# Kernel optimization log

Hardware: AMD Instinct MI355X
Metric: run time of the kernel (lower is better)

## Reference

```python
import jax, jax.numpy as jnp
import numpy as np

EPS = 1e-12  # torch F.normalize default eps


def _l2norm(x):
    n = jnp.linalg.norm(x, axis=-1, keepdims=True)
    return x / jnp.maximum(n, EPS)


def setup_inputs() -> dict:
    key = jax.random.key(0)
    k1, k2 = jax.random.split(key)
    B, D = 8192, 1024
    img_emb = jax.random.normal(k1, (B, D), dtype=jnp.float32)
    txt_emb = jax.random.normal(k2, (B, D), dtype=jnp.float32)
    t_prime = jnp.asarray(np.log(1.0 / 0.1), dtype=jnp.float32)  # log(1/temperature_init)
    bias = jnp.asarray(-10.0, dtype=jnp.float32)
    return {"img_emb": img_emb, "txt_emb": txt_emb, "t_prime": t_prime, "bias": bias}


def reference(img_emb, txt_emb, t_prime, bias):
    img = _l2norm(img_emb)
    txt = _l2norm(txt_emb)
    t = jnp.minimum(jnp.exp(t_prime), 100.0)
    logits = jnp.einsum('id,jd->ij', img, txt) * t + bias  # [B, B]
    B = img.shape[0]
    # STANDARD mode: labels = 2*I - 1
    labels = 2.0 * jnp.eye(B, dtype=logits.dtype) - 1.0
    loss = -jnp.sum(jax.nn.log_sigmoid(labels * logits)) / B
    return loss
```

## Files before the change

kernel.cpp:

```cpp
#include <hip/hip_runtime.h>
#include <hip/hip_bf16.h>

#define B_SZ 8192
#define D_SZ 1024

typedef __attribute__((ext_vector_type(4))) float floatx4;
typedef __attribute__((ext_vector_type(8))) int   int8v;
typedef __attribute__((ext_vector_type(4))) int   int4v;

__device__ __forceinline__ void glds16(const void* g, void* l) {
    __builtin_amdgcn_global_load_lds(
        (const __attribute__((address_space(1))) void*)g,
        (__attribute__((address_space(3))) void*)l, 16, 0, 0);
}

__global__ __launch_bounds__(256) void norm_cast_fp8(
    const float* __restrict__ img, const float* __restrict__ txt,
    unsigned char* __restrict__ imgQ, unsigned char* __restrict__ txtQ)
{
    const int lane = threadIdx.x & 63;
    int w = blockIdx.x * 4 + (threadIdx.x >> 6);
    const float* src; unsigned char* dst;
    if (w < B_SZ) { src = img + (size_t)w * D_SZ; dst = imgQ + (size_t)w * D_SZ; }
    else { w -= B_SZ; src = txt + (size_t)w * D_SZ; dst = txtQ + (size_t)w * D_SZ; }

    float4 v[4];
    float ss = 0.0f;
    #pragma unroll
    for (int i = 0; i < 4; ++i) {
        v[i] = ((const float4*)src)[lane + 64 * i];
        ss += v[i].x*v[i].x + v[i].y*v[i].y + v[i].z*v[i].z + v[i].w*v[i].w;
    }
    #pragma unroll
    for (int off = 1; off < 64; off <<= 1) ss += __shfl_xor(ss, off, 64);
    const float scale = 1.0f / fmaxf(sqrtf(ss), 1e-12f);

    #pragma unroll
    for (int i = 0; i < 4; ++i) {
        int packed = 0;
        packed = __builtin_amdgcn_cvt_pk_fp8_f32(v[i].x * scale, v[i].y * scale, packed, false);
        packed = __builtin_amdgcn_cvt_pk_fp8_f32(v[i].z * scale, v[i].w * scale, packed, true);
        ((int*)dst)[lane + 64 * i] = packed;
    }
}

__global__ __launch_bounds__(256, 3) void siglip_gemm_loss_fp8(
    const unsigned char* __restrict__ A,
    const unsigned char* __restrict__ Bt,
    const float* __restrict__ tp, const float* __restrict__ bp,
    float* __restrict__ out)
{
    __shared__ __align__(16) unsigned char As[2][128 * 64];
    __shared__ __align__(16) unsigned char Bs[2][128 * 64];

    const int tid  = threadIdx.x;
    const int lane = tid & 63;
    const int wave = tid >> 6;
    const int wm = wave & 1, wn = wave >> 1;
    const int bi = blockIdx.x * 128;
    const int bj = blockIdx.y * 128;
    const int quad = lane >> 4;
    const int l16  = lane & 15;

    floatx4 acc[4][4];
    #pragma unroll
    for (int i = 0; i < 4; ++i)
        #pragma unroll
        for (int j = 0; j < 4; ++j)
            acc[i][j] = (floatx4){0.f, 0.f, 0.f, 0.f};

    auto stage = [&](int k0) {
        #pragma unroll
        for (int it = 0; it < 2; ++it) {
            int s = tid + it * 256;
            int row = s >> 2, p = s & 3;
            int g = p ^ ((row >> 1) & 3);
            const unsigned char* ga = A  + ((size_t)(bi + row) * D_SZ + k0 + g * 16);
            const unsigned char* gb = Bt + ((size_t)(bj + row) * D_SZ + k0 + g * 16);
            glds16(ga,      As[0] + s * 16);
            glds16(ga + 64, As[1] + s * 16);
            glds16(gb,      Bs[0] + s * 16);
            glds16(gb + 64, Bs[1] + s * 16);
        }
    };

    const int sw = (l16 >> 1) & 3;
    const int hsel = quad >> 1;
    const int q2 = (quad & 1) * 2;
    const int p0 = (q2    ) ^ sw;
    const int p1 = (q2 + 1) ^ sw;

    stage(0);

    for (int kk = 0; kk < D_SZ / 128; ++kk) {
        __syncthreads();

        int8v af[4], bf[4];
        #pragma unroll
        for (int mt = 0; mt < 4; ++mt) {
            int r = wm * 64 + mt * 16 + l16;
            int4v lo = *(const int4v*)(As[hsel] + r * 64 + p0 * 16);
            int4v hi = *(const int4v*)(As[hsel] + r * 64 + p1 * 16);
            af[mt][0]=lo[0]; af[mt][1]=lo[1]; af[mt][2]=lo[2]; af[mt][3]=lo[3];
            af[mt][4]=hi[0]; af[mt][5]=hi[1]; af[mt][6]=hi[2]; af[mt][7]=hi[3];
        }
        #pragma unroll
        for (int nt = 0; nt < 4; ++nt) {
            int r = wn * 64 + nt * 16 + l16;
            int4v lo = *(const int4v*)(Bs[hsel] + r * 64 + p0 * 16);
            int4v hi = *(const int4v*)(Bs[hsel] + r * 64 + p1 * 16);
            bf[nt][0]=lo[0]; bf[nt][1]=lo[1]; bf[nt][2]=lo[2]; bf[nt][3]=lo[3];
            bf[nt][4]=hi[0]; bf[nt][5]=hi[1]; bf[nt][6]=hi[2]; bf[nt][7]=hi[3];
        }

        __syncthreads();

        if (kk + 1 < D_SZ / 128)
            stage((kk + 1) * 128);

        #pragma unroll
        for (int mt = 0; mt < 4; ++mt)
            #pragma unroll
            for (int nt = 0; nt < 4; ++nt)
                acc[mt][nt] = __builtin_amdgcn_mfma_scale_f32_16x16x128_f8f6f4(
                    af[mt], bf[nt], acc[mt][nt],
                    0, 0,
                    0, 127,
                    0, 127);
    }

    const float t    = fminf(__expf(tp[0]), 100.0f);
    const float bias = bp[0];
    float lsum = 0.0f;
    #pragma unroll
    for (int mt = 0; mt < 4; ++mt) {
        #pragma unroll
        for (int nt = 0; nt < 4; ++nt) {
            const int jj = bj + wn * 64 + nt * 16 + l16;
            #pragma unroll
            for (int r = 0; r < 4; ++r) {
                const int ii = bi + wm * 64 + mt * 16 + quad * 4 + r;
                float logit = fmaf(acc[mt][nt][r], t, bias);
                float z = (ii == jj) ? logit : -logit;
                float e = __expf(-fabsf(z));
                lsum += fmaxf(-z, 0.0f) + __logf(1.0f + e);
            }
        }
    }
    #pragma unroll
    for (int off = 32; off > 0; off >>= 1) lsum += __shfl_down(lsum, off, 64);

    __shared__ float red[4];
    if (lane == 0) red[wave] = lsum;
    __syncthreads();
    if (tid == 0)
        atomicAdd(out, (red[0] + red[1] + red[2] + red[3]) * (1.0f / (float)B_SZ));
}

extern "C" void kernel_launch(void* const* d_in, const int* in_sizes, int n_in,
                              void* d_out, int out_size, void* d_ws, size_t ws_size,
                              hipStream_t stream) {
    const float* img = (const float*)d_in[0];
    const float* txt = (const float*)d_in[1];
    const float* tp  = (const float*)d_in[2];
    const float* bp  = (const float*)d_in[3];
    float* out = (float*)d_out;

    unsigned char* imgQ = (unsigned char*)d_ws;
    unsigned char* txtQ = imgQ + (size_t)B_SZ * D_SZ;

    hipMemsetAsync(out, 0, sizeof(float), stream);
    norm_cast_fp8<<<(2 * B_SZ) / 4, 256, 0, stream>>>(img, txt, imgQ, txtQ);
    dim3 grid(B_SZ / 128, B_SZ / 128);
    siglip_gemm_loss_fp8<<<grid, 256, 0, stream>>>(imgQ, txtQ, tp, bp, out);
}
```

Baseline: 192.3 us.

## Enlarge GEMM tile to 256x128, double-buffer A, fold output zeroing into norm kernel

The fused GEMM+loss kernel now computes a 256x128 output tile per block, with each wave holding an 8x4 grid of MFMA accumulators. A fragments are streamed from LDS inside the MFMA loop, and the A tile is double-buffered in LDS. The goal is more reuse of each B fragment and fewer global loads per FLOP. The launch bound drops to 2 blocks per SM to fit the larger register and LDS footprint, and the grid is halved. The separate memset is removed and the output is zeroed inside the norm kernel, which saves one launch.

After: 229.7 us. +19.5%, slower.

```diff
diff --git a/kernel.cpp b/kernel.cpp
--- a/kernel.cpp
+++ b/kernel.cpp
@@ -16,8 +16,11 @@
 
 __global__ __launch_bounds__(256) void norm_cast_fp8(
     const float* __restrict__ img, const float* __restrict__ txt,
-    unsigned char* __restrict__ imgQ, unsigned char* __restrict__ txtQ)
+    unsigned char* __restrict__ imgQ, unsigned char* __restrict__ txtQ,
+    float* __restrict__ out)
 {
+    if (blockIdx.x == 0 && threadIdx.x == 0) *out = 0.0f;
+
     const int lane = threadIdx.x & 63;
     int w = blockIdx.x * 4 + (threadIdx.x >> 6);
     const float* src; unsigned char* dst;
@@ -44,102 +47,111 @@
     }
 }
 
-__global__ __launch_bounds__(256, 3) void siglip_gemm_loss_fp8(
+__global__ __launch_bounds__(256, 2) void siglip_gemm_loss_fp8(
     const unsigned char* __restrict__ A,
     const unsigned char* __restrict__ Bt,
     const float* __restrict__ tp, const float* __restrict__ bp,
     float* __restrict__ out)
 {
-    __shared__ __align__(16) unsigned char As[2][128 * 64];
+    __shared__ __align__(16) unsigned char As[2][2][256 * 64];
     __shared__ __align__(16) unsigned char Bs[2][128 * 64];
 
     const int tid  = threadIdx.x;
     const int lane = tid & 63;
     const int wave = tid >> 6;
     const int wm = wave & 1, wn = wave >> 1;
-    const int bi = blockIdx.x * 128;
+    const int bi = blockIdx.x * 256;
     const int bj = blockIdx.y * 128;
     const int quad = lane >> 4;
     const int l16  = lane & 15;
 
-    floatx4 acc[4][4];
+    floatx4 acc[8][4];
     #pragma unroll
-    for (int i = 0; i < 4; ++i)
+    for (int i = 0; i < 8; ++i)
         #pragma unroll
         for (int j = 0; j < 4; ++j)
             acc[i][j] = (floatx4){0.f, 0.f, 0.f, 0.f};
 
-    auto stage = [&](int k0) {
+    auto stage_a = [&](int k0, int buf) {
+        #pragma unroll
+        for (int it = 0; it < 4; ++it) {
+            int s = tid + it * 256;
+            int row = s >> 2, p = s & 3;
+            int g = p ^ ((row >> 1) & 3);
+            const unsigned char* ga = A + ((size_t)(bi + row) * D_SZ + k0 + g * 16);
+            glds16(ga,      As[buf][0] + s * 16);
+            glds16(ga + 64, As[buf][1] + s * 16);
+        }
+    };
+    auto stage_b = [&](int k0) {
         #pragma unroll
         for (int it = 0; it < 2; ++it) {
             int s = tid + it * 256;
             int row = s >> 2, p = s & 3;
             int g = p ^ ((row >> 1) & 3);
-            const unsigned char* ga = A  + ((size_t)(bi + row) * D_SZ + k0 + g * 16);
             const unsigned char* gb = Bt + ((size_t)(bj + row) * D_SZ + k0 + g * 16);
-            glds16(ga,      As[0] + s * 16);
-            glds16(ga + 64, As[1] + s * 16);
             glds16(gb,      Bs[0] + s * 16);
             glds16(gb + 64, Bs[1] + s * 16);
         }
     };
 
-    const int sw = (l16 >> 1) & 3;
+    const int sw   = (l16 >> 1) & 3;
     const int hsel = quad >> 1;
-    const int q2 = (quad & 1) * 2;
-    const int p0 = (q2    ) ^ sw;
-    const int p1 = (q2 + 1) ^ sw;
+    const int p0   = ((quad & 1) * 2) ^ sw;
+    const int p1   = p0 ^ 1;
 
-    stage(0);
+    stage_a(0, 0);
+    stage_b(0);
 
     for (int kk = 0; kk < D_SZ / 128; ++kk) {
         __syncthreads();
+        const int buf = kk & 1;
 
-        int8v af[4], bf[4];
-        #pragma unroll
-        for (int mt = 0; mt < 4; ++mt) {
-            int r = wm * 64 + mt * 16 + l16;
-            int4v lo = *(const int4v*)(As[hsel] + r * 64 + p0 * 16);
-            int4v hi = *(const int4v*)(As[hsel] + r * 64 + p1 * 16);
-            af[mt][0]=lo[0]; af[mt][1]=lo[1]; af[mt][2]=lo[2]; af[mt][3]=lo[3];
-            af[mt][4]=hi[0]; af[mt][5]=hi[1]; af[mt][6]=hi[2]; af[mt][7]=hi[3];
-        }
+        int8v bfr[4];
         #pragma unroll
         for (int nt = 0; nt < 4; ++nt) {
             int r = wn * 64 + nt * 16 + l16;
             int4v lo = *(const int4v*)(Bs[hsel] + r * 64 + p0 * 16);
             int4v hi = *(const int4v*)(Bs[hsel] + r * 64 + p1 * 16);
-            bf[nt][0]=lo[0]; bf[nt][1]=lo[1]; bf[nt][2]=lo[2]; bf[nt][3]=lo[3];
-            bf[nt][4]=hi[0]; bf[nt][5]=hi[1]; bf[nt][6]=hi[2]; bf[nt][7]=hi[3];
+            bfr[nt][0]=lo[0]; bfr[nt][1]=lo[1]; bfr[nt][2]=lo[2]; bfr[nt][3]=lo[3];
+            bfr[nt][4]=hi[0]; bfr[nt][5]=hi[1]; bfr[nt][6]=hi[2]; bfr[nt][7]=hi[3];
+        }
+        __syncthreads();
+
+        if (kk + 1 < D_SZ / 128) {
+            stage_a((kk + 1) * 128, buf ^ 1);
+            stage_b((kk + 1) * 128);
         }
 
-        __syncthreads();
-
-        if (kk + 1 < D_SZ / 128)
-            stage((kk + 1) * 128);
-
         #pragma unroll
-        for (int mt = 0; mt < 4; ++mt)
+        for (int mt = 0; mt < 8; ++mt) {
+            int r = wm * 128 + mt * 16 + l16;
+            int4v lo = *(const int4v*)(As[buf][hsel] + r * 64 + p0 * 16);
+            int4v hi = *(const int4v*)(As[buf][hsel] + r * 64 + p1 * 16);
+            int8v af;
+            af[0]=lo[0]; af[1]=lo[1]; af[2]=lo[2]; af[3]=lo[3];
+            af[4]=hi[0]; af[5]=hi[1]; af[6]=hi[2]; af[7]=hi[3];
             #pragma unroll
             for (int nt = 0; nt < 4; ++nt)
                 acc[mt][nt] = __builtin_amdgcn_mfma_scale_f32_16x16x128_f8f6f4(
-                    af[mt], bf[nt], acc[mt][nt],
+                    af, bfr[nt], acc[mt][nt],
                     0, 0,
                     0, 127,
                     0, 127);
+        }
     }
 
     const float t    = fminf(__expf(tp[0]), 100.0f);
     const float bias = bp[0];
     float lsum = 0.0f;
     #pragma unroll
-    for (int mt = 0; mt < 4; ++mt) {
+    for (int mt = 0; mt < 8; ++mt) {
         #pragma unroll
         for (int nt = 0; nt < 4; ++nt) {
             const int jj = bj + wn * 64 + nt * 16 + l16;
             #pragma unroll
             for (int r = 0; r < 4; ++r) {
-                const int ii = bi + wm * 64 + mt * 16 + quad * 4 + r;
+                const int ii = bi + wm * 128 + mt * 16 + quad * 4 + r;
                 float logit = fmaf(acc[mt][nt][r], t, bias);
                 float z = (ii == jj) ? logit : -logit;
                 float e = __expf(-fabsf(z));
@@ -169,8 +181,7 @@
     unsigned char* imgQ = (unsigned char*)d_ws;
     unsigned char* txtQ = imgQ + (size_t)B_SZ * D_SZ;
 
-    hipMemsetAsync(out, 0, sizeof(float), stream);
-    norm_cast_fp8<<<(2 * B_SZ) / 4, 256, 0, stream>>>(img, txt, imgQ, txtQ);
-    dim3 grid(B_SZ / 128, B_SZ / 128);
+    norm_cast_fp8<<<(2 * B_SZ) / 4, 256, 0, stream>>>(img, txt, imgQ, txtQ, out);
+    dim3 grid(B_SZ / 256, B_SZ / 128);
     siglip_gemm_loss_fp8<<<grid, 256, 0, stream>>>(imgQ, txtQ, tp, bp, out);
 }
```

## Load A fragments directly from global memory and fold output zeroing into norm kernel

Applied to the files above, without the earlier changes.

The A operand tile is no longer staged through LDS. Each lane loads its 32-byte fp8 fragment straight from global memory into registers every k-step, so only B goes through LDS. This halves LDS traffic and footprint, which may allow more occupancy. The trade-off is uncoalesced, latency-exposed global loads that are issued right before the MFMAs with no prefetch. Separately, the output is zeroed inside the norm kernel instead of by a hipMemsetAsync, which saves one launch.

New measurement: 258.0 us. 1.34x slower.

```diff
diff --git a/kernel.cpp b/kernel.cpp
--- a/kernel.cpp
+++ b/kernel.cpp
@@ -16,8 +16,11 @@
 
 __global__ __launch_bounds__(256) void norm_cast_fp8(
     const float* __restrict__ img, const float* __restrict__ txt,
-    unsigned char* __restrict__ imgQ, unsigned char* __restrict__ txtQ)
+    unsigned char* __restrict__ imgQ, unsigned char* __restrict__ txtQ,
+    float* __restrict__ out)
 {
+    if (blockIdx.x == 0 && threadIdx.x == 0) *out = 0.0f;
+
     const int lane = threadIdx.x & 63;
     int w = blockIdx.x * 4 + (threadIdx.x >> 6);
     const float* src; unsigned char* dst;
@@ -50,7 +53,6 @@
     const float* __restrict__ tp, const float* __restrict__ bp,
     float* __restrict__ out)
 {
-    __shared__ __align__(16) unsigned char As[2][128 * 64];
     __shared__ __align__(16) unsigned char Bs[2][128 * 64];
 
     const int tid  = threadIdx.x;
@@ -69,61 +71,61 @@
         for (int j = 0; j < 4; ++j)
             acc[i][j] = (floatx4){0.f, 0.f, 0.f, 0.f};
 
-    auto stage = [&](int k0) {
+    auto stage_b = [&](int k0) {
         #pragma unroll
         for (int it = 0; it < 2; ++it) {
             int s = tid + it * 256;
             int row = s >> 2, p = s & 3;
             int g = p ^ ((row >> 1) & 3);
-            const unsigned char* ga = A  + ((size_t)(bi + row) * D_SZ + k0 + g * 16);
             const unsigned char* gb = Bt + ((size_t)(bj + row) * D_SZ + k0 + g * 16);
-            glds16(ga,      As[0] + s * 16);
-            glds16(ga + 64, As[1] + s * 16);
             glds16(gb,      Bs[0] + s * 16);
             glds16(gb + 64, Bs[1] + s * 16);
         }
     };
 
-    const int sw = (l16 >> 1) & 3;
+    const int sw   = (l16 >> 1) & 3;
     const int hsel = quad >> 1;
-    const int q2 = (quad & 1) * 2;
-    const int p0 = (q2    ) ^ sw;
-    const int p1 = (q2 + 1) ^ sw;
+    const int p0   = ((quad & 1) * 2) ^ sw;
+    const int p1   = p0 ^ 1;
 
-    stage(0);
+    const unsigned char* a_lane = A + (size_t)(bi + l16) * D_SZ + quad * 32;
+
+    stage_b(0);
 
     for (int kk = 0; kk < D_SZ / 128; ++kk) {
         __syncthreads();
 
-        int8v af[4], bf[4];
-        #pragma unroll
-        for (int mt = 0; mt < 4; ++mt) {
-            int r = wm * 64 + mt * 16 + l16;
-            int4v lo = *(const int4v*)(As[hsel] + r * 64 + p0 * 16);
-            int4v hi = *(const int4v*)(As[hsel] + r * 64 + p1 * 16);
-            af[mt][0]=lo[0]; af[mt][1]=lo[1]; af[mt][2]=lo[2]; af[mt][3]=lo[3];
-            af[mt][4]=hi[0]; af[mt][5]=hi[1]; af[mt][6]=hi[2]; af[mt][7]=hi[3];
-        }
+        int8v bfr[4];
         #pragma unroll
         for (int nt = 0; nt < 4; ++nt) {
             int r = wn * 64 + nt * 16 + l16;
             int4v lo = *(const int4v*)(Bs[hsel] + r * 64 + p0 * 16);
             int4v hi = *(const int4v*)(Bs[hsel] + r * 64 + p1 * 16);
-            bf[nt][0]=lo[0]; bf[nt][1]=lo[1]; bf[nt][2]=lo[2]; bf[nt][3]=lo[3];
-            bf[nt][4]=hi[0]; bf[nt][5]=hi[1]; bf[nt][6]=hi[2]; bf[nt][7]=hi[3];
+            bfr[nt][0]=lo[0]; bfr[nt][1]=lo[1]; bfr[nt][2]=lo[2]; bfr[nt][3]=lo[3];
+            bfr[nt][4]=hi[0]; bfr[nt][5]=hi[1]; bfr[nt][6]=hi[2]; bfr[nt][7]=hi[3];
         }
-
         __syncthreads();
 
         if (kk + 1 < D_SZ / 128)
-            stage((kk + 1) * 128);
+            stage_b((kk + 1) * 128);
+
+        const unsigned char* ak = a_lane + (size_t)(wm * 64) * D_SZ + kk * 128;
+        int8v af[4];
+        #pragma unroll
+        for (int mt = 0; mt < 4; ++mt) {
+            const unsigned char* ap = ak + (size_t)(mt * 16) * D_SZ;
+            int4v lo = *(const int4v*)(ap);
+            int4v hi = *(const int4v*)(ap + 16);
+            af[mt][0]=lo[0]; af[mt][1]=lo[1]; af[mt][2]=lo[2]; af[mt][3]=lo[3];
+            af[mt][4]=hi[0]; af[mt][5]=hi[1]; af[mt][6]=hi[2]; af[mt][7]=hi[3];
+        }
 
         #pragma unroll
         for (int mt = 0; mt < 4; ++mt)
             #pragma unroll
             for (int nt = 0; nt < 4; ++nt)
                 acc[mt][nt] = __builtin_amdgcn_mfma_scale_f32_16x16x128_f8f6f4(
-                    af[mt], bf[nt], acc[mt][nt],
+                    af[mt], bfr[nt], acc[mt][nt],
                     0, 0,
                     0, 127,
                     0, 127);
@@ -169,8 +171,7 @@
     unsigned char* imgQ = (unsigned char*)d_ws;
     unsigned char* txtQ = imgQ + (size_t)B_SZ * D_SZ;
 
-    hipMemsetAsync(out, 0, sizeof(float), stream);
-    norm_cast_fp8<<<(2 * B_SZ) / 4, 256, 0, stream>>>(img, txt, imgQ, txtQ);
+    norm_cast_fp8<<<(2 * B_SZ) / 4, 256, 0, stream>>>(img, txt, imgQ, txtQ, out);
     dim3 grid(B_SZ / 128, B_SZ / 128);
     siglip_gemm_loss_fp8<<<grid, 256, 0, stream>>>(imgQ, txtQ, tp, bp, out);
 }
```
